# Performance work log

Measured on AMD Instinct MI355X. Metric: run time of the kernel, lower is better.

The kernel has to match this reference:

```python
import jax, jax.numpy as jnp
import numpy as np

B, S, D = 1, 2048, 2048
H = 16
HD = D // H           # 128
FFN_H = 5632          # int(2*4*D/3) rounded up to multiple of 256
EPS = 1e-5
ROPE_THETA = 10000.0


def rms_norm(x, w, eps=EPS):
    # x * rsqrt(mean(x^2, -1) + eps) * w
    return x * jax.lax.rsqrt(jnp.mean(x * x, axis=-1, keepdims=True) + eps) * w


def apply_rope(x, cos, sin):
    # x: [B, S, H, HD]; cos/sin: [S, HD//2]
    b, s, h, hd = x.shape
    xr = x.reshape(b, s, h, hd // 2, 2)
    x_re, x_im = xr[..., 0], xr[..., 1]
    c = cos[None, :, None, :]
    sn = sin[None, :, None, :]
    o_re = x_re * c - x_im * sn
    o_im = x_re * sn + x_im * c
    return jnp.stack([o_re, o_im], axis=-1).reshape(b, s, h, hd)


def setup_inputs() -> dict:
    key = jax.random.key(0)
    ks = jax.random.split(key, 10)
    x = jax.random.normal(ks[0], (B, S, D), dtype=jnp.float32)
    # RoPE frequencies (Llama-style)
    inv_freq = 1.0 / (ROPE_THETA ** (np.arange(0, HD, 2, dtype=np.float32) / HD))
    angles = np.outer(np.arange(S, dtype=np.float32), inv_freq)  # [S, HD//2]
    freqs_cos = jnp.asarray(np.cos(angles), dtype=jnp.float32)
    freqs_sin = jnp.asarray(np.sin(angles), dtype=jnp.float32)
    # causal mask: 1 = keep, 0 = masked
    mask = jnp.tril(jnp.ones((S, S), dtype=jnp.int32))[None, None]
    sc = 0.02
    return {
        "x": x,
        "freqs_cos": freqs_cos,
        "freqs_sin": freqs_sin,
        "mask": mask,
        "wq": jax.random.normal(ks[1], (D, D), jnp.float32) * sc,
        "wk": jax.random.normal(ks[2], (D, D), jnp.float32) * sc,
        "wv": jax.random.normal(ks[3], (D, D), jnp.float32) * sc,
        "wo": jax.random.normal(ks[4], (D, D), jnp.float32) * sc,
        "w1": jax.random.normal(ks[5], (D, FFN_H), jnp.float32) * sc,
        "w2": jax.random.normal(ks[6], (FFN_H, D), jnp.float32) * sc,
        "w3": jax.random.normal(ks[7], (D, FFN_H), jnp.float32) * sc,
        "attn_norm_w": jnp.ones((D,), jnp.float32),
        "ffn_norm_w": jnp.ones((D,), jnp.float32),
    }


def reference(x, freqs_cos, freqs_sin, mask, wq, wk, wv, wo, w1, w2, w3,
              attn_norm_w, ffn_norm_w):
    b, s, d = x.shape
    # --- attention block ---
    xn = rms_norm(x, attn_norm_w)
    q = (xn @ wq).reshape(b, s, H, HD)
    k = (xn @ wk).reshape(b, s, H, HD)
    v = (xn @ wv).reshape(b, s, H, HD)
    q = apply_rope(q, freqs_cos, freqs_sin)
    k = apply_rope(k, freqs_cos, freqs_sin)
    scores = jnp.einsum('bqhd,bkhd->bhqk', q, k) / jnp.sqrt(jnp.float32(HD))
    scores = jnp.where(mask == 0, -jnp.inf, scores)
    probs = jax.nn.softmax(scores, axis=-1)
    attn = jnp.einsum('bhqk,bkhd->bqhd', probs, v).reshape(b, s, d)
    h = x + attn @ wo
    # --- SwiGLU FFN block ---
    hn = rms_norm(h, ffn_norm_w)
    ff = (jax.nn.silu(hn @ w1) * (hn @ w3)) @ w2
    return h + ff
```

## Files before the change

kernel.cpp:

```cpp
#include <hip/hip_runtime.h>
#include <hip/hip_bf16.h>

typedef __bf16 bf16x8 __attribute__((ext_vector_type(8)));
typedef float f32x4 __attribute__((ext_vector_type(4)));
typedef unsigned short u16x8 __attribute__((ext_vector_type(8)));
typedef unsigned short u16x4 __attribute__((ext_vector_type(4)));

#define DEV static __device__ __forceinline__

DEV unsigned short f2bf(float f) {
    unsigned u = __builtin_bit_cast(unsigned, f);
    u += 0x7fffu + ((u >> 16) & 1u);
    return (unsigned short)(u >> 16);
}
DEV float bf2f(unsigned short h) {
    unsigned u = ((unsigned)h) << 16;
    return __builtin_bit_cast(float, u);
}

DEV void gl2lds16(const void* g, void* l) {
    __builtin_amdgcn_global_load_lds(
        (const __attribute__((address_space(1))) void*)g,
        (__attribute__((address_space(3))) void*)l, 16, 0, 0);
}

#define WAITV(N) asm volatile("s_waitcnt vmcnt(" #N ")" ::: "memory")
#define SBAR()   asm volatile("s_barrier" ::: "memory")

#define STAGE32(KT, BUF)                                                      \
    _Pragma("unroll")                                                         \
    for (int sl = 0; sl < 3; ++sl) {                                          \
        const unsigned short* sbase = (sl == 0)                               \
            ? A  + (size_t)bm * K                                             \
            : BT + (size_t)(bn + (sl - 1) * 128) * K;                         \
        const unsigned short* g = sbase + (size_t)srow * K                    \
                                  + koff + (KT) * 32 + lc;                    \
        gl2lds16(g, &lds[BUF][sl][wave * 512]);                               \
    }

#define DSREAD32(BUF, AR, BR)                                                 \
    {                                                                         \
        const char* Ab = (const char*)&lds[BUF][0][0];                        \
        const char* Bb = (const char*)&lds[BUF][1 + (wn >> 1)][0];            \
        _Pragma("unroll")                                                     \
        for (int m4 = 0; m4 < 4; ++m4) {                                      \
            const int rw = wm * 64 + m4 * 16 + lr;                            \
            AR[m4] = *(const bf16x8*)(Ab + rw * 64 +                          \
                     ((lg * 16) ^ (((rw >> 1) & 3) << 4)));                   \
        }                                                                     \
        _Pragma("unroll")                                                     \
        for (int n2 = 0; n2 < 4; ++n2) {                                      \
            const int rw = (wn & 1) * 64 + n2 * 16 + lr;                      \
            BR[n2] = *(const bf16x8*)(Bb + rw * 64 +                          \
                     ((lg * 16) ^ (((rw >> 1) & 3) << 4)));                   \
        }                                                                     \
    }

#define MFMA16(AR, BR)                                                        \
    __builtin_amdgcn_s_setprio(1);                                            \
    _Pragma("unroll")                                                         \
    for (int m4 = 0; m4 < 4; ++m4)                                            \
        _Pragma("unroll")                                                     \
        for (int n2 = 0; n2 < 4; ++n2)                                        \
            acc[m4][n2] = __builtin_amdgcn_mfma_f32_16x16x32_bf16(            \
                AR[m4], BR[n2], acc[m4][n2], 0, 0, 0);                        \
    __builtin_amdgcn_s_setprio(0);

template <int EPI>
__global__ __launch_bounds__(512, 4)
void gemm128d(const unsigned short* __restrict__ A,
              const unsigned short* __restrict__ BT,
              unsigned short* __restrict__ outB,
              float* __restrict__ outP,
              int M, int N, int K,
              const float* __restrict__ cs, const float* __restrict__ sn,
              unsigned short* __restrict__ vT)
{
    __shared__ alignas(16) unsigned short lds[3][3][4096];
    const int tid  = threadIdx.x;
    const int lane = tid & 63;
    const int wave = tid >> 6;
    const int wm = wave >> 2;
    const int wn = wave & 3;
    const int lr = lane & 15;
    const int lg = lane >> 4;
    const int gy  = gridDim.y;
    const int lin = blockIdx.y * gridDim.x + blockIdx.x;
    const int cpx = (gridDim.x * gy) >> 3;
    const int swz = (lin & 7) * cpx + (lin >> 3);
    const int bm = (swz % gy) * 128;
    const int bn = (swz / gy) * 256;
    const int srow = tid >> 2;
    const int lc   = (((tid & 3) ^ ((srow >> 1) & 3)) << 3);
    int koff, NT;
    if constexpr (EPI == 1 || EPI == 3) {
        const int Kh = K >> 1; koff = blockIdx.z * Kh; NT = Kh >> 5;
    } else {
        koff = 0; NT = K >> 5;
    }

    f32x4 acc[4][4] = {};
    bf16x8 a_[4], b_[4];

    STAGE32(0, 0);
    STAGE32(1, 1);
    WAITV(3); SBAR();
    DSREAD32(0, a_, b_);

    int bc = 0;
    for (int kt = 0; kt < NT - 2; ++kt) {
        const int nb = (bc == 0) ? 2 : bc - 1;
        STAGE32(kt + 2, nb);
        MFMA16(a_, b_);
        WAITV(3); SBAR();
        const int rb = (bc == 2) ? 0 : bc + 1;
        DSREAD32(rb, a_, b_);
        bc = rb;
    }
    MFMA16(a_, b_);
    WAITV(0); SBAR();
    {
        const int rb = (bc == 2) ? 0 : bc + 1;
        DSREAD32(rb, a_, b_);
    }
    MFMA16(a_, b_);

#pragma unroll
    for (int m4 = 0; m4 < 4; ++m4) {
        const int row = bm + wm * 64 + m4 * 16 + lg * 4;
#pragma unroll
        for (int n2 = 0; n2 < 4; ++n2) {
            const int col = bn + wn * 64 + n2 * 16 + lr;
            if constexpr (EPI == 4) {
                if (bn >= 4096) {
                    u16x4 o;
#pragma unroll
                    for (int r = 0; r < 4; ++r) o[r] = f2bf(acc[m4][n2][r]);
                    *(u16x4*)(vT + (size_t)(col - 4096) * 2048 + row) = o;
                } else {
#pragma unroll
                    for (int r = 0; r < 4; ++r) {
                        const float v  = acc[m4][n2][r];
                        const float vo = __shfl_xor(v, 1);
                        const int rr = row + r;
                        const int i0 = (col & 127) >> 1;
                        const float c = cs[rr * 64 + i0];
                        const float s = sn[rr * 64 + i0];
                        const float o = (lr & 1) ? (vo * s + v * c)
                                                 : (v * c - vo * s);
                        outB[(size_t)rr * N + col] = f2bf(o);
                    }
                }
            } else {
#pragma unroll
                for (int r = 0; r < 4; ++r) {
                    if constexpr (EPI == 0) {
                        outB[(size_t)(row + r) * N + col] = f2bf(acc[m4][n2][r]);
                    } else if constexpr (EPI == 1) {
                        outP[(size_t)blockIdx.z * M * N + (size_t)(row + r) * N + col] = acc[m4][n2][r];
                    } else if constexpr (EPI == 3) {
                        unsafeAtomicAdd(&outP[(size_t)(row + r) * N + col], acc[m4][n2][r]);
                    } else {
                        const float v  = acc[m4][n2][r];
                        const float vo = __shfl_xor(v, 1);
                        const float x1 = (lr & 1) ? vo : v;
                        const float x3 = (lr & 1) ? v : vo;
                        const float g  = x1 / (1.0f + __expf(-x1)) * x3;
                        if (!(lr & 1))
                            outB[(size_t)(row + r) * (N >> 1) + (col >> 1)] = f2bf(g);
                    }
                }
            }
        }
    }
}

__global__ __launch_bounds__(256)
void reduce2_norm(const float* __restrict__ res, const float* __restrict__ p,
                  const float* __restrict__ w, float* __restrict__ hout,
                  unsigned short* __restrict__ nout)
{
    const int row = blockIdx.x, tid = threadIdx.x;
    const float4* r4 = (const float4*)(res + (size_t)row * 2048);
    const float4* a4 = (const float4*)(p   + (size_t)row * 2048);
    const float4* b4 = (const float4*)(p + (size_t)2048 * 2048 + (size_t)row * 2048);
    float4* h4 = (float4*)(hout + (size_t)row * 2048);
    float4 h[2];
    float ss = 0.f;
#pragma unroll
    for (int i = 0; i < 2; ++i) {
        const int idx = i * 256 + tid;
        const float4 r = r4[idx], a = a4[idx], b = b4[idx];
        float4 v = make_float4(r.x + a.x + b.x, r.y + a.y + b.y,
                               r.z + a.z + b.z, r.w + a.w + b.w);
        h[i] = v; h4[idx] = v;
        ss += v.x * v.x + v.y * v.y + v.z * v.z + v.w * v.w;
    }
#pragma unroll
    for (int off = 32; off; off >>= 1) ss += __shfl_xor(ss, off);
    __shared__ float red[4];
    if ((tid & 63) == 0) red[tid >> 6] = ss;
    __syncthreads();
    const float tot = red[0] + red[1] + red[2] + red[3];
    const float sc = rsqrtf(tot * (1.0f / 2048.0f) + 1e-5f);
#pragma unroll
    for (int i = 0; i < 2; ++i) {
        const int idx = i * 256 + tid;
        const float4 wv = ((const float4*)w)[idx];
        u16x4 o;
        o[0] = f2bf(h[i].x * sc * wv.x); o[1] = f2bf(h[i].y * sc * wv.y);
        o[2] = f2bf(h[i].z * sc * wv.z); o[3] = f2bf(h[i].w * sc * wv.w);
        *(u16x4*)(nout + (size_t)row * 2048 + idx * 4) = o;
    }
}

__global__ __launch_bounds__(256)
void rmsnorm_kernel(const float* __restrict__ x, const float* __restrict__ w,
                    unsigned short* __restrict__ out)
{
    const int row = blockIdx.x;
    const int tid = threadIdx.x;
    const float* xr = x + (size_t)row * 2048;
    const float4 a = *reinterpret_cast<const float4*>(xr + tid * 8);
    const float4 b = *reinterpret_cast<const float4*>(xr + tid * 8 + 4);
    float ss = a.x * a.x + a.y * a.y + a.z * a.z + a.w * a.w
             + b.x * b.x + b.y * b.y + b.z * b.z + b.w * b.w;
#pragma unroll
    for (int off = 32; off; off >>= 1) ss += __shfl_xor(ss, off);
    __shared__ float red[4];
    if ((tid & 63) == 0) red[tid >> 6] = ss;
    __syncthreads();
    const float tot = red[0] + red[1] + red[2] + red[3];
    const float sc = rsqrtf(tot * (1.0f / 2048.0f) + 1e-5f);
    const float4 wa = *reinterpret_cast<const float4*>(w + tid * 8);
    const float4 wb = *reinterpret_cast<const float4*>(w + tid * 8 + 4);
    u16x8 o;
    o[0] = f2bf(a.x * sc * wa.x); o[1] = f2bf(a.y * sc * wa.y);
    o[2] = f2bf(a.z * sc * wa.z); o[3] = f2bf(a.w * sc * wa.w);
    o[4] = f2bf(b.x * sc * wb.x); o[5] = f2bf(b.y * sc * wb.y);
    o[6] = f2bf(b.z * sc * wb.z); o[7] = f2bf(b.w * sc * wb.w);
    *reinterpret_cast<u16x8*>(out + (size_t)row * 2048 + tid * 8) = o;
}

DEV void convT_body(const float* __restrict__ w, unsigned short* __restrict__ wT,
                    int K, int N, int rmul, int radd, int bk, int bn, int tid)
{
    __shared__ unsigned short t[64][66];
    const int r = tid >> 4, c4 = (tid & 15) * 4;
#pragma unroll
    for (int i = 0; i < 4; ++i) {
        const int row = r + i * 16;
        const float4 v = *reinterpret_cast<const float4*>(w + (size_t)(bk + row) * N + bn + c4);
        t[row][c4 + 0] = f2bf(v.x); t[row][c4 + 1] = f2bf(v.y);
        t[row][c4 + 2] = f2bf(v.z); t[row][c4 + 3] = f2bf(v.w);
    }
    __syncthreads();
#pragma unroll
    for (int i = 0; i < 4; ++i) {
        const int n = r + i * 16;
        u16x4 o;
#pragma unroll
        for (int e = 0; e < 4; ++e) o[e] = t[c4 + e][n];
        *reinterpret_cast<u16x4*>(wT + (size_t)(rmul * (bn + n) + radd) * K + bk + c4) = o;
    }
}

__global__ __launch_bounds__(256)
void convT_kernel(const float* __restrict__ w, unsigned short* __restrict__ wT,
                  int K, int N)
{
    convT_body(w, wT, K, N, 1, 0, blockIdx.y * 64, blockIdx.x * 64, threadIdx.x);
}

__global__ __launch_bounds__(256)
void convT4_kernel(const float* __restrict__ w0, const float* __restrict__ w1,
                   const float* __restrict__ w2, const float* __restrict__ w3,
                   unsigned short* __restrict__ wT)
{
    const int z = blockIdx.z;
    const float* w = (z == 0) ? w0 : (z == 1) ? w1 : (z == 2) ? w2 : w3;
    convT_body(w, wT + (size_t)z * 2048 * 2048, 2048, 2048, 1, 0,
               blockIdx.y * 64, blockIdx.x * 64, threadIdx.x);
}

__global__ __launch_bounds__(256)
void convTpair_kernel(const float* __restrict__ wa, const float* __restrict__ wb,
                      unsigned short* __restrict__ wT)
{
    const int z = blockIdx.z;
    convT_body(z ? wb : wa, wT, 2048, 5632, 2, z,
               blockIdx.y * 64, blockIdx.x * 64, threadIdx.x);
}

__global__ __launch_bounds__(512)
void flash_attn(const unsigned short* __restrict__ q,
                const unsigned short* __restrict__ k,
                const unsigned short* __restrict__ vT,
                unsigned short* __restrict__ attn)
{
    __shared__ alignas(16) unsigned short Ks[2][64][136];
    __shared__ alignas(16) unsigned short Vs[2][128][72];
    __shared__ alignas(16) unsigned short Ps[8][16][72];

    const int hh = blockIdx.y;
    const int pi = blockIdx.x;
    const int tid = threadIdx.x;
    const int lane = tid & 63, wave = tid >> 6;
    const int qt = (wave >> 2) ? (31 - pi) : pi;
    const int lr = lane & 15, lg = lane >> 4;
    const int q0 = qt * 64 + (wave & 3) * 16;
    const int myNT = qt + 1;
    const int NT   = 32 - pi;

    const int kr0 = tid >> 4, kc0 = (tid & 15) * 8;
    const int vr0 = tid >> 3, vc0 = (tid & 7) * 8;

    bf16x8 qf[4];
#pragma unroll
    for (int c = 0; c < 4; ++c)
        qf[c] = *reinterpret_cast<const bf16x8*>(
            q + (size_t)(q0 + lr) * 6144 + hh * 128 + c * 32 + lg * 8);

    f32x4 oacc[8] = {};
    float m_r[4], l_r[4];
#pragma unroll
    for (int r = 0; r < 4; ++r) { m_r[r] = -INFINITY; l_r[r] = 0.0f; }
    const float scale = 0.08838834764831845f;

    u16x8 kreg0, kreg1, vreg0, vreg1;
    auto gload = [&](int kt) {
        const int kv0 = kt * 64;
        kreg0 = *reinterpret_cast<const u16x8*>(k + (size_t)(kv0 + kr0) * 6144 + hh * 128 + kc0);
        kreg1 = *reinterpret_cast<const u16x8*>(k + (size_t)(kv0 + kr0 + 32) * 6144 + hh * 128 + kc0);
        vreg0 = *reinterpret_cast<const u16x8*>(vT + (size_t)(hh * 128 + vr0) * 2048 + kv0 + vc0);
        vreg1 = *reinterpret_cast<const u16x8*>(vT + (size_t)(hh * 128 + vr0 + 64) * 2048 + kv0 + vc0);
    };
    auto lwrite = [&](int buf) {
        *reinterpret_cast<u16x8*>(&Ks[buf][kr0][kc0])      = kreg0;
        *reinterpret_cast<u16x8*>(&Ks[buf][kr0 + 32][kc0]) = kreg1;
        *reinterpret_cast<u16x8*>(&Vs[buf][vr0][vc0])      = vreg0;
        *reinterpret_cast<u16x8*>(&Vs[buf][vr0 + 64][vc0]) = vreg1;
    };

    gload(0); lwrite(0);
    __syncthreads();

    for (int kt = 0; kt < NT; ++kt) {
        const int buf = kt & 1;
        if (kt + 1 < NT) gload(kt + 1);

        if (kt < myNT) {
            const int kv0 = kt * 64;
            const bool masked = (kt == myNT - 1);
            f32x4 s[4] = {};
            __builtin_amdgcn_s_setprio(1);
#pragma unroll
            for (int ct = 0; ct < 4; ++ct)
#pragma unroll
                for (int c = 0; c < 4; ++c) {
                    const bf16x8 kf = *reinterpret_cast<const bf16x8*>(
                        &Ks[buf][ct * 16 + lr][c * 32 + lg * 8]);
                    s[ct] = __builtin_amdgcn_mfma_f32_16x16x32_bf16(qf[c], kf, s[ct], 0, 0, 0);
                }
            __builtin_amdgcn_s_setprio(0);
#pragma unroll
            for (int ct = 0; ct < 4; ++ct)
#pragma unroll
                for (int r = 0; r < 4; ++r) {
                    float v = s[ct][r] * scale;
                    if (masked) {
                        const int kvg = kv0 + ct * 16 + lr;
                        const int qg  = q0 + lg * 4 + r;
                        if (kvg > qg) v = -INFINITY;
                    }
                    s[ct][r] = v;
                }
            float mn[4], alpha[4], rs[4];
#pragma unroll
            for (int r = 0; r < 4; ++r) {
                float v = fmaxf(fmaxf(s[0][r], s[1][r]), fmaxf(s[2][r], s[3][r]));
                v = fmaxf(v, __shfl_xor(v, 1));
                v = fmaxf(v, __shfl_xor(v, 2));
                v = fmaxf(v, __shfl_xor(v, 4));
                v = fmaxf(v, __shfl_xor(v, 8));
                mn[r] = fmaxf(m_r[r], v);
                alpha[r] = __expf(m_r[r] - mn[r]);
                m_r[r] = mn[r];
                rs[r] = 0.0f;
            }
#pragma unroll
            for (int ct = 0; ct < 4; ++ct)
#pragma unroll
                for (int r = 0; r < 4; ++r) {
                    const float p = __expf(s[ct][r] - mn[r]);
                    s[ct][r] = p;
                    rs[r] += p;
                }
#pragma unroll
            for (int r = 0; r < 4; ++r) {
                float t2 = rs[r];
                t2 += __shfl_xor(t2, 1);
                t2 += __shfl_xor(t2, 2);
                t2 += __shfl_xor(t2, 4);
                t2 += __shfl_xor(t2, 8);
                l_r[r] = l_r[r] * alpha[r] + t2;
            }
#pragma unroll
            for (int ot = 0; ot < 8; ++ot)
#pragma unroll
                for (int r = 0; r < 4; ++r) oacc[ot][r] *= alpha[r];

#pragma unroll
            for (int ct = 0; ct < 4; ++ct)
#pragma unroll
                for (int r = 0; r < 4; ++r)
                    Ps[wave][lg * 4 + r][ct * 16 + lr] = f2bf(s[ct][r]);

            __builtin_amdgcn_s_setprio(1);
#pragma unroll
            for (int c2 = 0; c2 < 2; ++c2) {
                const bf16x8 pf = *reinterpret_cast<const bf16x8*>(
                    &Ps[wave][lr][c2 * 32 + lg * 8]);
#pragma unroll
                for (int ot = 0; ot < 8; ++ot) {
                    const bf16x8 vf = *reinterpret_cast<const bf16x8*>(
                        &Vs[buf][ot * 16 + lr][c2 * 32 + lg * 8]);
                    oacc[ot] = __builtin_amdgcn_mfma_f32_16x16x32_bf16(pf, vf, oacc[ot], 0, 0, 0);
                }
            }
            __builtin_amdgcn_s_setprio(0);
        }

        if (kt + 1 < NT) lwrite(buf ^ 1);
        __syncthreads();
    }

#pragma unroll
    for (int ot = 0; ot < 8; ++ot)
#pragma unroll
        for (int r = 0; r < 4; ++r) {
            const float v = oacc[ot][r] / l_r[r];
            attn[(size_t)(q0 + lg * 4 + r) * 2048 + hh * 128 + ot * 16 + lr] = f2bf(v);
        }
}

extern "C" void kernel_launch(void* const* d_in, const int* in_sizes, int n_in,
                              void* d_out, int out_size, void* d_ws, size_t ws_size,
                              hipStream_t stream)
{
    const float* x    = (const float*)d_in[0];
    const float* fcos = (const float*)d_in[1];
    const float* fsin = (const float*)d_in[2];
    const float* wq  = (const float*)d_in[4];
    const float* wk  = (const float*)d_in[5];
    const float* wv  = (const float*)d_in[6];
    const float* wo  = (const float*)d_in[7];
    const float* w1  = (const float*)d_in[8];
    const float* w2  = (const float*)d_in[9];
    const float* w3  = (const float*)d_in[10];
    const float* anw = (const float*)d_in[11];
    const float* fnw = (const float*)d_in[12];
    float* out = (float*)d_out;

    char* ws = (char*)d_ws;
    size_t off = 0;
    auto alloc = [&](size_t bytes) { void* p = ws + off; off += bytes; return p; };
    const size_t SZ_DD = (size_t)2048 * 2048 * 2;
    const size_t SZ_DF = (size_t)2048 * 5632 * 2;

    unsigned short* qkvoT = (unsigned short*)alloc(4 * SZ_DD);
    unsigned short* w13T  = (unsigned short*)alloc(2 * SZ_DF);
    unsigned short* w2T   = (unsigned short*)alloc(SZ_DF);

    char* reg1 = (char*)alloc((size_t)48 * 1024 * 1024);
    unsigned short* xn   = (unsigned short*)reg1;
    unsigned short* qkv  = (unsigned short*)(reg1 + SZ_DD);
    unsigned short* vTb  = (unsigned short*)(reg1 + SZ_DD + 3 * SZ_DD);
    unsigned short* ab   = (unsigned short*)(reg1 + SZ_DD + 4 * SZ_DD);
    float*          pk   = (float*)reg1;
    unsigned short* hn   = (unsigned short*)(reg1 + 4 * SZ_DD);

    char* reg2 = (char*)alloc(SZ_DF);
    unsigned short* t1 = (unsigned short*)reg2;

    convT4_kernel<<<dim3(32, 32, 4), 256, 0, stream>>>(wq, wk, wv, wo, qkvoT);
    convTpair_kernel<<<dim3(88, 32, 2), 256, 0, stream>>>(w1, w3, w13T);
    convT_kernel<<<dim3(32, 88), 256, 0, stream>>>(w2, w2T, 5632, 2048);

    rmsnorm_kernel<<<2048, 256, 0, stream>>>(x, anw, xn);
    gemm128d<4><<<dim3(24, 16), 512, 0, stream>>>(xn, qkvoT, qkv, nullptr,
                                                  2048, 6144, 2048, fcos, fsin, vTb);
    flash_attn<<<dim3(16, 16), 512, 0, stream>>>(qkv, qkv + 2048, vTb, ab);
    gemm128d<1><<<dim3(8, 16, 2), 512, 0, stream>>>(ab, qkvoT + 3 * (size_t)2048 * 2048,
                                                    nullptr, pk, 2048, 2048, 2048,
                                                    nullptr, nullptr, nullptr);
    reduce2_norm<<<2048, 256, 0, stream>>>(x, pk, fnw, out, hn);

    gemm128d<2><<<dim3(44, 16), 512, 0, stream>>>(hn, w13T, t1, nullptr,
                                                  2048, 11264, 2048,
                                                  nullptr, nullptr, nullptr);
    gemm128d<3><<<dim3(8, 16, 2), 512, 0, stream>>>(t1, w2T, nullptr, out,
                                                    2048, 2048, 5632,
                                                    nullptr, nullptr, nullptr);
}
```

Baseline: 440.6 us.

## Fuse fp32 weight conversion and transpose into GEMM B-operand loading

```diff
diff --git a/kernel.cpp b/kernel.cpp
--- a/kernel.cpp
+++ b/kernel.cpp
@@ -25,17 +25,48 @@
 }
 
 #define WAITV(N) asm volatile("s_waitcnt vmcnt(" #N ")" ::: "memory")
+#define WAITL()  asm volatile("s_waitcnt lgkmcnt(0)" ::: "memory")
 #define SBAR()   asm volatile("s_barrier" ::: "memory")
 
-#define STAGE32(KT, BUF)                                                      \
+#define STAGEA(KT, BUF)                                                       \
+    {                                                                         \
+        const unsigned short* g = A + (size_t)(bm + srow) * K                 \
+                                  + koff + (KT) * 32 + lc;                    \
+        gl2lds16(g, &lds[BUF][0][wave * 512]);                                \
+    }
+
+#define LOADB(KT, BR)                                                         \
     _Pragma("unroll")                                                         \
-    for (int sl = 0; sl < 3; ++sl) {                                          \
-        const unsigned short* sbase = (sl == 0)                               \
-            ? A  + (size_t)bm * K                                             \
-            : BT + (size_t)(bn + (sl - 1) * 128) * K;                         \
-        const unsigned short* g = sbase + (size_t)srow * K                    \
-                                  + koff + (KT) * 32 + lc;                    \
-        gl2lds16(g, &lds[BUF][sl][wave * 512]);                               \
+    for (int rp = 0; rp < 2; ++rp) {                                          \
+        const int u  = tid + 512 * rp;                                        \
+        const int nn = u & 255;                                               \
+        const int kc = u >> 8;                                                \
+        const float* bsrc; int bcol; int bstr;                                \
+        if constexpr (BMODE == 0) { bsrc = B0; bcol = bn + nn; bstr = N; }    \
+        else if constexpr (BMODE == 1) {                                      \
+            const int sel = bn >> 11;                                         \
+            bsrc = sel == 0 ? B0 : (sel == 1 ? B1 : B2);                      \
+            bcol = (bn + nn) & 2047; bstr = 2048;                             \
+        } else {                                                              \
+            bsrc = (nn & 1) ? B1 : B0; bcol = (bn + nn) >> 1; bstr = 5632;    \
+        }                                                                     \
+        _Pragma("unroll")                                                     \
+        for (int i = 0; i < 8; ++i)                                           \
+            BR[rp][i] = bsrc[(size_t)(koff + (KT) * 32 + kc * 8 + i) * bstr + bcol]; \
+    }
+
+#define WRITEB(BR, BUF)                                                       \
+    _Pragma("unroll")                                                         \
+    for (int rp = 0; rp < 2; ++rp) {                                          \
+        const int u  = tid + 512 * rp;                                        \
+        const int nn = u & 255;                                               \
+        const int kc = u >> 8;                                                \
+        const int rw = nn & 127;                                              \
+        u16x8 pkv;                                                            \
+        _Pragma("unroll")                                                     \
+        for (int i = 0; i < 8; ++i) pkv[i] = f2bf(BR[rp][i]);                 \
+        *(u16x8*)(&lds[BUF][1 + (nn >> 7)]                                    \
+                     [rw * 32 + ((kc * 8) ^ (((rw >> 1) & 3) << 3))]) = pkv;  \
     }
 
 #define DSREAD32(BUF, AR, BR)                                                 \
@@ -66,10 +97,12 @@
                 AR[m4], BR[n2], acc[m4][n2], 0, 0, 0);                        \
     __builtin_amdgcn_s_setprio(0);
 
-template <int EPI>
-__global__ __launch_bounds__(512, 4)
+template <int EPI, int BMODE>
+__global__ __launch_bounds__(512, 2)
 void gemm128d(const unsigned short* __restrict__ A,
-              const unsigned short* __restrict__ BT,
+              const float* __restrict__ B0,
+              const float* __restrict__ B1,
+              const float* __restrict__ B2,
               unsigned short* __restrict__ outB,
               float* __restrict__ outP,
               int M, int N, int K,
@@ -101,26 +134,46 @@
 
     f32x4 acc[4][4] = {};
     bf16x8 a_[4], b_[4];
-
-    STAGE32(0, 0);
-    STAGE32(1, 1);
-    WAITV(3); SBAR();
+    float brE[2][8], brO[2][8];
+
+    STAGEA(0, 0); LOADB(0, brE);
+    STAGEA(1, 1); LOADB(1, brO);
+    WAITV(17);
+    WRITEB(brE, 0);
+    WAITL(); SBAR();
     DSREAD32(0, a_, b_);
 
     int bc = 0;
-    for (int kt = 0; kt < NT - 2; ++kt) {
-        const int nb = (bc == 0) ? 2 : bc - 1;
-        STAGE32(kt + 2, nb);
-        MFMA16(a_, b_);
-        WAITV(3); SBAR();
-        const int rb = (bc == 2) ? 0 : bc + 1;
-        DSREAD32(rb, a_, b_);
-        bc = rb;
+    for (int kt = 0; kt + 3 < NT; kt += 2) {
+        {
+            const int nb = (bc == 0) ? 2 : bc - 1;
+            STAGEA(kt + 2, nb); LOADB(kt + 2, brE);
+            MFMA16(a_, b_);
+            WAITV(17);
+            const int rb = (bc == 2) ? 0 : bc + 1;
+            WRITEB(brO, rb);
+            WAITL(); SBAR();
+            DSREAD32(rb, a_, b_);
+            bc = rb;
+        }
+        {
+            const int nb = (bc == 0) ? 2 : bc - 1;
+            STAGEA(kt + 3, nb); LOADB(kt + 3, brO);
+            MFMA16(a_, b_);
+            WAITV(17);
+            const int rb = (bc == 2) ? 0 : bc + 1;
+            WRITEB(brE, rb);
+            WAITL(); SBAR();
+            DSREAD32(rb, a_, b_);
+            bc = rb;
+        }
     }
     MFMA16(a_, b_);
-    WAITV(0); SBAR();
+    WAITV(0);
     {
         const int rb = (bc == 2) ? 0 : bc + 1;
+        WRITEB(brO, rb);
+        WAITL(); SBAR();
         DSREAD32(rb, a_, b_);
     }
     MFMA16(a_, b_);
@@ -154,9 +207,7 @@
             } else {
 #pragma unroll
                 for (int r = 0; r < 4; ++r) {
-                    if constexpr (EPI == 0) {
-                        outB[(size_t)(row + r) * N + col] = f2bf(acc[m4][n2][r]);
-                    } else if constexpr (EPI == 1) {
+                    if constexpr (EPI == 1) {
                         outP[(size_t)blockIdx.z * M * N + (size_t)(row + r) * N + col] = acc[m4][n2][r];
                     } else if constexpr (EPI == 3) {
                         unsafeAtomicAdd(&outP[(size_t)(row + r) * N + col], acc[m4][n2][r]);
@@ -240,56 +291,6 @@
     o[4] = f2bf(b.x * sc * wb.x); o[5] = f2bf(b.y * sc * wb.y);
     o[6] = f2bf(b.z * sc * wb.z); o[7] = f2bf(b.w * sc * wb.w);
     *reinterpret_cast<u16x8*>(out + (size_t)row * 2048 + tid * 8) = o;
-}
-
-DEV void convT_body(const float* __restrict__ w, unsigned short* __restrict__ wT,
-                    int K, int N, int rmul, int radd, int bk, int bn, int tid)
-{
-    __shared__ unsigned short t[64][66];
-    const int r = tid >> 4, c4 = (tid & 15) * 4;
-#pragma unroll
-    for (int i = 0; i < 4; ++i) {
-        const int row = r + i * 16;
-        const float4 v = *reinterpret_cast<const float4*>(w + (size_t)(bk + row) * N + bn + c4);
-        t[row][c4 + 0] = f2bf(v.x); t[row][c4 + 1] = f2bf(v.y);
-        t[row][c4 + 2] = f2bf(v.z); t[row][c4 + 3] = f2bf(v.w);
-    }
-    __syncthreads();
-#pragma unroll
-    for (int i = 0; i < 4; ++i) {
-        const int n = r + i * 16;
-        u16x4 o;
-#pragma unroll
-        for (int e = 0; e < 4; ++e) o[e] = t[c4 + e][n];
-        *reinterpret_cast<u16x4*>(wT + (size_t)(rmul * (bn + n) + radd) * K + bk + c4) = o;
-    }
-}
-
-__global__ __launch_bounds__(256)
-void convT_kernel(const float* __restrict__ w, unsigned short* __restrict__ wT,
-                  int K, int N)
-{
-    convT_body(w, wT, K, N, 1, 0, blockIdx.y * 64, blockIdx.x * 64, threadIdx.x);
-}
-
-__global__ __launch_bounds__(256)
-void convT4_kernel(const float* __restrict__ w0, const float* __restrict__ w1,
-                   const float* __restrict__ w2, const float* __restrict__ w3,
-                   unsigned short* __restrict__ wT)
-{
-    const int z = blockIdx.z;
-    const float* w = (z == 0) ? w0 : (z == 1) ? w1 : (z == 2) ? w2 : w3;
-    convT_body(w, wT + (size_t)z * 2048 * 2048, 2048, 2048, 1, 0,
-               blockIdx.y * 64, blockIdx.x * 64, threadIdx.x);
-}
-
-__global__ __launch_bounds__(256)
-void convTpair_kernel(const float* __restrict__ wa, const float* __restrict__ wb,
-                      unsigned short* __restrict__ wT)
-{
-    const int z = blockIdx.z;
-    convT_body(z ? wb : wa, wT, 2048, 5632, 2, z,
-               blockIdx.y * 64, blockIdx.x * 64, threadIdx.x);
 }
 
 __global__ __launch_bounds__(512)
@@ -468,10 +469,6 @@
     const size_t SZ_DD = (size_t)2048 * 2048 * 2;
     const size_t SZ_DF = (size_t)2048 * 5632 * 2;
 
-    unsigned short* qkvoT = (unsigned short*)alloc(4 * SZ_DD);
-    unsigned short* w13T  = (unsigned short*)alloc(2 * SZ_DF);
-    unsigned short* w2T   = (unsigned short*)alloc(SZ_DF);
-
     char* reg1 = (char*)alloc((size_t)48 * 1024 * 1024);
     unsigned short* xn   = (unsigned short*)reg1;
     unsigned short* qkv  = (unsigned short*)(reg1 + SZ_DD);
@@ -483,23 +480,19 @@
     char* reg2 = (char*)alloc(SZ_DF);
     unsigned short* t1 = (unsigned short*)reg2;
 
-    convT4_kernel<<<dim3(32, 32, 4), 256, 0, stream>>>(wq, wk, wv, wo, qkvoT);
-    convTpair_kernel<<<dim3(88, 32, 2), 256, 0, stream>>>(w1, w3, w13T);
-    convT_kernel<<<dim3(32, 88), 256, 0, stream>>>(w2, w2T, 5632, 2048);
-
     rmsnorm_kernel<<<2048, 256, 0, stream>>>(x, anw, xn);
-    gemm128d<4><<<dim3(24, 16), 512, 0, stream>>>(xn, qkvoT, qkv, nullptr,
-                                                  2048, 6144, 2048, fcos, fsin, vTb);
+    gemm128d<4, 1><<<dim3(24, 16), 512, 0, stream>>>(
+        xn, wq, wk, wv, qkv, nullptr, 2048, 6144, 2048, fcos, fsin, vTb);
     flash_attn<<<dim3(16, 16), 512, 0, stream>>>(qkv, qkv + 2048, vTb, ab);
-    gemm128d<1><<<dim3(8, 16, 2), 512, 0, stream>>>(ab, qkvoT + 3 * (size_t)2048 * 2048,
-                                                    nullptr, pk, 2048, 2048, 2048,
-                                                    nullptr, nullptr, nullptr);
+    gemm128d<1, 0><<<dim3(8, 16, 2), 512, 0, stream>>>(
+        ab, wo, nullptr, nullptr, nullptr, pk, 2048, 2048, 2048,
+        nullptr, nullptr, nullptr);
     reduce2_norm<<<2048, 256, 0, stream>>>(x, pk, fnw, out, hn);
 
-    gemm128d<2><<<dim3(44, 16), 512, 0, stream>>>(hn, w13T, t1, nullptr,
-                                                  2048, 11264, 2048,
-                                                  nullptr, nullptr, nullptr);
-    gemm128d<3><<<dim3(8, 16, 2), 512, 0, stream>>>(t1, w2T, nullptr, out,
-                                                    2048, 2048, 5632,
-                                                    nullptr, nullptr, nullptr);
-}
+    gemm128d<2, 2><<<dim3(44, 16), 512, 0, stream>>>(
+        hn, w1, w3, nullptr, t1, nullptr, 2048, 11264, 2048,
+        nullptr, nullptr, nullptr);
+    gemm128d<3, 0><<<dim3(8, 16, 2), 512, 0, stream>>>(
+        t1, w2, nullptr, nullptr, nullptr, out, 2048, 2048, 5632,
+        nullptr, nullptr, nullptr);
+}
```

New measurement: 733.9 us. 1.67x slower.
